# Performance work log

Hardware: AMD Instinct MI355X
Metric: run time of the kernel (lower is better)

## Reference

```python
import jax, jax.numpy as jnp
import numpy as np

N = 100_000   # nodes
E = 1_600_000 # edges
D_IN = 64
HID = 512
OUT = 64
NSEG = HID // OUT  # 8
P = [0, 1, 2]
BN_EPS = 1e-5


def setup_inputs() -> dict:
    key = jax.random.key(0)
    ks = jax.random.split(key, 16)
    feats = jax.random.normal(ks[0], (N, D_IN), dtype=jnp.float32)
    src = jax.random.randint(ks[1], (E,), 0, N, dtype=jnp.int32)
    dst = jax.random.randint(ks[2], (E,), 0, N, dtype=jnp.int32)
    s_in = 1.0 / np.sqrt(D_IN)
    s_fc = 1.0 / np.sqrt(HID * len(P))
    W0 = jax.random.uniform(ks[3], (HID, D_IN), jnp.float32, -s_in, s_in)
    b0 = jnp.zeros((HID,), jnp.float32)
    W1 = jax.random.uniform(ks[4], (HID, D_IN), jnp.float32, -s_in, s_in)
    b1 = jnp.zeros((HID,), jnp.float32)
    W2 = jax.random.uniform(ks[5], (HID, D_IN), jnp.float32, -s_in, s_in)
    b2 = jnp.zeros((HID,), jnp.float32)
    fc_W = jax.random.uniform(ks[6], (HID, HID * len(P)), jnp.float32, -s_fc, s_fc)
    fc_b = jnp.zeros((HID,), jnp.float32)
    gamma = jnp.ones((HID,), jnp.float32)
    beta = jnp.zeros((HID,), jnp.float32)
    q = jax.random.uniform(ks[7], (NSEG,), jnp.float32)
    return dict(feats=feats, src=src, dst=dst, W0=W0, b0=b0, W1=W1, b1=b1,
                W2=W2, b2=b2, fc_W=fc_W, fc_b=fc_b, gamma=gamma, beta=beta, q=q)


def _mixhop_layer(feats, src, dst, Ws, bs, fc_W, fc_b, gamma, beta):
    # degree norm: deg^{-1/2}, clamped at 1
    deg = jax.ops.segment_sum(jnp.ones((E,), feats.dtype), dst, num_segments=N)
    norm = jnp.clip(deg, 1.0, None) ** -0.5  # [N]
    norm = norm[:, None]
    outputs = []
    h = feats
    for j in range(max(P) + 1):
        h = h * norm
        # SpMM: sum over incoming edges (copy_u + sum)
        h = jax.ops.segment_sum(h[src], dst, num_segments=N)
        h = h * norm
        if j in P:
            outputs.append(h @ Ws[j].T + bs[j])  # [N, HID]
    cat = jnp.concatenate(outputs, axis=1)       # [N, 3*HID]
    final = cat @ fc_W.T + fc_b                  # [N, HID]
    # BatchNorm1d (training-mode batch statistics, biased var)
    mu = jnp.mean(final, axis=0)
    var = jnp.mean((final - mu) ** 2, axis=0)
    final = (final - mu) * jax.lax.rsqrt(var + BN_EPS) * gamma + beta
    return final


def reference(feats, src, dst, W0, b0, W1, b1, W2, b2, fc_W, fc_b, gamma, beta, q):
    h = _mixhop_layer(feats, src, dst, [W0, W1, W2], [b0, b1, b2],
                      fc_W, fc_b, gamma, beta)           # [N, HID]
    # segment mixing: sum_k q[k] * h[:, k*OUT:(k+1)*OUT]
    out = jnp.einsum('nko,k->no', h.reshape(N, NSEG, OUT), q)  # [N, OUT]
    return out
```

## Files before the change

kernel.cpp:

```cpp
#include <hip/hip_runtime.h>
#include <hip/hip_bf16.h>
#include <stdint.h>

typedef unsigned short ushort;
typedef unsigned int uint;
typedef unsigned char uchar;

#define N_NODES 100000
#define N_EDGES 1600000
#define KDIM 192
#define HIDDEN 512
#define NCHUNK 782
#define NCH 2
#define NPART 391
#define SDIM (KDIM*KDIM)
#define NPAIR 78
#define PPB   9984
#define NSPLIT 8
#define LDT 194
#define NSLICE 256
#define EPS (N_EDGES/NSLICE)

#define NB 391
#define BCAP 5120

typedef __attribute__((ext_vector_type(8))) short short8;
typedef __attribute__((ext_vector_type(4))) short short4v;
typedef __attribute__((ext_vector_type(4))) uint uint4v;
typedef __attribute__((ext_vector_type(4))) float float4v;
typedef __attribute__((ext_vector_type(2))) float float2v;
typedef __attribute__((ext_vector_type(2))) uint uint2v;

__device__ __forceinline__ float bf2f(ushort u){
    uint x = ((uint)u) << 16;
    return __builtin_bit_cast(float, x);
}
__device__ __forceinline__ float bflo(uint u){
    return __builtin_bit_cast(float, u << 16);
}
__device__ __forceinline__ float bfhi(uint u){
    return __builtin_bit_cast(float, u & 0xffff0000u);
}
__device__ __forceinline__ ushort f2bf(float f){
    uint u = __builtin_bit_cast(uint, f);
    u += 0x7fffu + ((u >> 16) & 1u);
    return (ushort)(u >> 16);
}

__global__ __launch_bounds__(1024) void k_histA(const int* __restrict__ dst,
                                                uint* __restrict__ histA){
    __shared__ uint cnt[NB];
    int slice = blockIdx.x, t = threadIdx.x;
    for (int b = t; b < NB; b += 1024) cnt[b] = 0;
    __syncthreads();
    int e0 = slice * EPS;
    for (int i = t; i < EPS; i += 1024){
        uint d = (uint)dst[e0 + i];
        atomicAdd(&cnt[d >> 8], 1u);
    }
    __syncthreads();
    for (int b = t; b < NB; b += 1024) histA[(size_t)b*NSLICE + slice] = cnt[b];
}

__global__ void k_scanSl(const uint* __restrict__ histA, uint* __restrict__ sbase,
                         uint* __restrict__ btot){
    __shared__ uint sc[NSLICE];
    int b = blockIdx.x, t = threadIdx.x;
    uint v = histA[(size_t)b*NSLICE + t];
    sc[t] = v; __syncthreads();
    for (int off = 1; off < 256; off <<= 1){
        uint u = (t >= off) ? sc[t - off] : 0;
        __syncthreads();
        sc[t] += u;
        __syncthreads();
    }
    sbase[(size_t)b*NSLICE + t] = sc[t] - v;
    if (t == 255) btot[b] = sc[255];
}

__global__ void k_scanBk(const uint* __restrict__ btot, uint* __restrict__ bstart){
    __shared__ uint sc[512];
    int t = threadIdx.x;
    uint v = (t < NB) ? btot[t] : 0;
    sc[t] = v; __syncthreads();
    for (int off = 1; off < 512; off <<= 1){
        uint u = (t >= off) ? sc[t - off] : 0;
        __syncthreads();
        sc[t] += u;
        __syncthreads();
    }
    if (t < NB) bstart[t] = sc[t] - v;
}

__global__ __launch_bounds__(1024) void k_packA(const int* __restrict__ src,
                                                const int* __restrict__ dst,
                                                const uint* __restrict__ sbase,
                                                const uint* __restrict__ bstart,
                                                uint* __restrict__ rec){
    __shared__ uint arr[NB];
    int slice = blockIdx.x, t = threadIdx.x;
    for (int b = t; b < NB; b += 1024)
        arr[b] = bstart[b] + sbase[(size_t)b*NSLICE + slice];
    __syncthreads();
    int e0 = slice * EPS;
    for (int i = t; i < EPS; i += 1024){
        int e = e0 + i;
        uint d = (uint)dst[e];
        uint bk = d >> 8;
        uint slot = atomicAdd(&arr[bk], 1u);
        rec[slot] = (uint)src[e] | ((d & 255u) << 17);
    }
}

__global__ __launch_bounds__(256) void k_passB(const uint* __restrict__ rec,
                                               const uint* __restrict__ bstart,
                                               const uint* __restrict__ btot,
                                               const float* __restrict__ feats,
                                               int* __restrict__ csr,
                                               int* __restrict__ deg,
                                               int* __restrict__ rowptr,
                                               float* __restrict__ nrm,
                                               ushort* __restrict__ Hx){
    __shared__ uint recs[BCAP];
    __shared__ uint cntL[256];
    __shared__ uint ofs[256];
    __shared__ float nrmL[256];
    int b = blockIdx.x, t = threadIdx.x;
    uint base = bstart[b], cnt = btot[b];
    cntL[t] = 0;
    __syncthreads();
    for (uint i = t; i < cnt; i += 256){
        uint rv = rec[base + i];
        if (i < BCAP) recs[i] = rv;
        atomicAdd(&cntL[(rv >> 17) & 255u], 1u);
    }
    __syncthreads();
    uint c = cntL[t];
    ofs[t] = c; __syncthreads();
    for (int off = 1; off < 256; off <<= 1){
        uint u = (t >= off) ? ofs[t - off] : 0;
        __syncthreads();
        ofs[t] += u;
        __syncthreads();
    }
    uint excl = ofs[t] - c;
    int node = b*256 + t;
    float nv = rsqrtf((float)(c > 0 ? c : 1));
    nrmL[t] = nv;
    if (node < N_NODES){
        deg[node] = (int)c;
        rowptr[node] = (int)(base + excl);
        nrm[node] = nv;
    }
    __syncthreads();
    ofs[t] = excl;
    __syncthreads();
    for (uint i = t; i < cnt; i += 256){
        uint rv = (i < BCAP) ? recs[i] : rec[base + i];
        uint n = (rv >> 17) & 255u;
        uint p = atomicAdd(&ofs[n], 1u);
        csr[base + p] = (int)(rv & 0x1FFFFu);
    }
    int nodeBase = b*256;
    for (int g = t; g < 256*16; g += 256){
        int ln = g >> 4;
        int nd = nodeBase + ln;
        if (nd < N_NODES){
            float w = nrmL[ln];
            float4v v = ((const float4v*)feats)[(long)nd*16 + (g & 15)];
            short4v o;
            o[0] = (short)f2bf(v[0]*w); o[1] = (short)f2bf(v[1]*w);
            o[2] = (short)f2bf(v[2]*w); o[3] = (short)f2bf(v[3]*w);
            ((short4v*)Hx)[(long)nd*16 + (g & 15)] = o;
        }
    }
}

template<bool WRITE_HS>
__global__ __launch_bounds__(256, 4) void k_agg(const ushort* __restrict__ inp,
                      ushort* __restrict__ H, int outoff,
                      ushort* __restrict__ Hs,
                      const int* __restrict__ rowptr, const int* __restrict__ deg,
                      const float* __restrict__ nrm, const int* __restrict__ csr){
    int node = (blockIdx.x << 3) + (threadIdx.x >> 5);
    int lane = threadIdx.x & 63;
    if (node >= N_NODES) return;
    int slot = (lane & 31) >> 3;
    int fb   = lane & 7;
    int beg = rowptr[node];
    int d   = deg[node];
    float acc[8] = {};
    if (d > 0 && d <= 32){
        int emax = beg + d - 1;
        int idx[8];
        #pragma unroll
        for (int k = 0; k < 8; ++k){
            int e = beg + slot + k*4;
            idx[k] = csr[e < emax ? e : emax];
        }
        uint4v v[8];
        #pragma unroll
        for (int k = 0; k < 8; ++k)
            v[k] = *(const uint4v*)(inp + (long)idx[k]*64 + fb*8);
        #pragma unroll
        for (int k = 0; k < 8; ++k){
            if (slot + k*4 < d){
                #pragma unroll
                for (int p = 0; p < 4; ++p){
                    acc[2*p]   += bflo(v[k][p]);
                    acc[2*p+1] += bfhi(v[k][p]);
                }
            }
        }
    } else if (d > 32){
        int i = 0;
        for (; i + 8 <= d; i += 8){
            int sA = csr[beg + i + slot];
            int sB = csr[beg + i + 4 + slot];
            uint4v vA = *(const uint4v*)(inp + (long)sA*64 + fb*8);
            uint4v vB = *(const uint4v*)(inp + (long)sB*64 + fb*8);
            #pragma unroll
            for (int p = 0; p < 4; ++p){
                acc[2*p]   += bflo(vA[p]); acc[2*p+1] += bfhi(vA[p]);
                acc[2*p]   += bflo(vB[p]); acc[2*p+1] += bfhi(vB[p]);
            }
        }
        if (i + 4 <= d){
            int sA = csr[beg + i + slot];
            uint4v vA = *(const uint4v*)(inp + (long)sA*64 + fb*8);
            #pragma unroll
            for (int p = 0; p < 4; ++p){
                acc[2*p]   += bflo(vA[p]); acc[2*p+1] += bfhi(vA[p]);
            }
            i += 4;
        }
        if (i + slot < d){
            int s = csr[beg + i + slot];
            uint4v v = *(const uint4v*)(inp + (long)s*64 + fb*8);
            #pragma unroll
            for (int p = 0; p < 4; ++p){
                acc[2*p]   += bflo(v[p]); acc[2*p+1] += bfhi(v[p]);
            }
        }
    }
    #pragma unroll
    for (int k = 0; k < 8; ++k){
        acc[k] += __shfl_xor(acc[k], 8);
        acc[k] += __shfl_xor(acc[k], 16);
    }
    if (slot == 0){
        float wn = nrm[node];
        short8 o;
        #pragma unroll
        for (int k = 0; k < 8; ++k) o[k] = (short)f2bf(wn * acc[k]);
        *(short8*)(H + (long)node*KDIM + outoff + fb*8) = o;
        if (WRITE_HS){
            float w2 = wn * wn;
            short8 o2;
            #pragma unroll
            for (int k = 0; k < 8; ++k) o2[k] = (short)f2bf(w2 * acc[k]);
            *(short8*)(Hs + (long)node*64 + fb*8) = o2;
        }
    }
}

__global__ __launch_bounds__(192) void k_prepM1(const float* __restrict__ W0,
                                                const float* __restrict__ W1,
                                                const float* __restrict__ W2,
                                                const float* __restrict__ fcW,
                                                float* __restrict__ MTp){
    int ks = blockIdx.x;
    int c0 = blockIdx.y * 4;
    int jd = threadIdx.x;
    int j = jd >> 6, d = jd & 63;
    const float* W  = (j == 0) ? W0 : (j == 1) ? W1 : W2;
    const float* wp = W + (ks*64)*64 + d;
    const float* f0 = fcW + (long)(c0+0)*1536 + j*512 + ks*64;
    const float* f1 = fcW + (long)(c0+1)*1536 + j*512 + ks*64;
    const float* f2 = fcW + (long)(c0+2)*1536 + j*512 + ks*64;
    const float* f3 = fcW + (long)(c0+3)*1536 + j*512 + ks*64;
    float a0 = 0.f, a1 = 0.f, a2 = 0.f, a3 = 0.f;
    #pragma unroll 8
    for (int k = 0; k < 64; ++k){
        float w = wp[k*64];
        a0 += w * f0[k]; a1 += w * f1[k]; a2 += w * f2[k]; a3 += w * f3[k];
    }
    long base = (long)ks*(HIDDEN*KDIM) + (long)c0*KDIM + jd;
    MTp[base]         = a0;
    MTp[base + KDIM]  = a1;
    MTp[base + 2*KDIM]= a2;
    MTp[base + 3*KDIM]= a3;
}

__global__ void k_prepM2(const float* __restrict__ MTp, ushort* __restrict__ MT){
    int i = blockIdx.x*256 + threadIdx.x;
    if (i >= HIDDEN*KDIM) return;
    float s = 0.f;
    #pragma unroll
    for (int ks = 0; ks < 8; ++ks) s += MTp[(long)ks*(HIDDEN*KDIM) + i];
    MT[i] = f2bf(s);
}

__global__ __launch_bounds__(256) void k_bias(const float* __restrict__ b0,
                                              const float* __restrict__ b1,
                                              const float* __restrict__ b2,
                                              const float* __restrict__ fcW,
                                              const float* __restrict__ fcb,
                                              float* __restrict__ Bc){
    __shared__ float red[256];
    int c = blockIdx.x, t = threadIdx.x;
    const float* fw = fcW + (long)c*1536;
    float s = b0[t]*fw[t]          + b0[t+256]*fw[t+256]
            + b1[t]*fw[512+t]      + b1[t+256]*fw[512+t+256]
            + b2[t]*fw[1024+t]     + b2[t+256]*fw[1024+t+256];
    red[t] = s; __syncthreads();
    for (int off = 128; off > 0; off >>= 1){
        if (t < off) red[t] += red[t + off];
        __syncthreads();
    }
    if (t == 0) Bc[c] = fcb[c] + red[0];
}

template<int W>
__device__ __forceinline__ void do_pairs(const short8* frag, float4v* acc){
    int p = 0, c = 0;
    #pragma unroll
    for (int i = 0; i < 12; ++i)
        #pragma unroll
        for (int j = i; j < 12; ++j){
            if ((p & 3) == W){
                acc[c] = __builtin_amdgcn_mfma_f32_16x16x32_bf16(frag[i], frag[j], acc[c], 0,0,0);
                ++c;
            }
            ++p;
        }
}
template<int W>
__device__ __forceinline__ void store_pairs(const float4v* acc, uint* Pb, int lane){
    int p = 0, c = 0;
    #pragma unroll
    for (int i = 0; i < 12; ++i)
        #pragma unroll
        for (int j = i; j < 12; ++j){
            if ((p & 3) == W){
                uint2v v;
                v[0] = (uint)f2bf(acc[c][0]) | ((uint)f2bf(acc[c][1]) << 16);
                v[1] = (uint)f2bf(acc[c][2]) | ((uint)f2bf(acc[c][3]) << 16);
                *(uint2v*)(Pb + p*128 + lane*2) = v;
                ++c;
            }
            ++p;
        }
}

__global__ __launch_bounds__(256, 2) void k_hth(const ushort* __restrict__ H,
                                                uint* __restrict__ P,
                                                float* __restrict__ msum){
    __shared__ ushort Ts[128*LDT];
    int t = threadIdx.x;
    int w = t >> 6, lane = t & 63;
    int m16 = lane & 15, quad = lane >> 4;
    float4v acc[20] = {};
    #pragma unroll
    for (int cc = 0; cc < NCH; ++cc){
        int chunk = blockIdx.x * NCH + cc;
        int n0 = chunk * 128;
        #pragma unroll
        for (int it = 0; it < 12; ++it){
            int flat = it*256 + t;
            int row = flat / 24, seg = flat - row*24;
            int gr = n0 + row;
            short8 v = {0,0,0,0,0,0,0,0};
            if (gr < N_NODES) v = *(const short8*)(H + (long)gr*KDIM + seg*8);
            *(short8*)(Ts + row*LDT + seg*8) = v;
        }
        __syncthreads();
        #pragma unroll
        for (int kt = 0; kt < 4; ++kt){
            short8 frag[12];
            #pragma unroll
            for (int b = 0; b < 12; ++b){
                short8 f;
                #pragma unroll
                for (int j = 0; j < 8; ++j)
                    f[j] = (short)Ts[(kt*32 + quad*8 + j)*LDT + b*16 + m16];
                frag[b] = f;
            }
            if      (w == 0) do_pairs<0>(frag, acc);
            else if (w == 1) do_pairs<1>(frag, acc);
            else if (w == 2) do_pairs<2>(frag, acc);
            else             do_pairs<3>(frag, acc);
        }
        if (t < KDIM){
            float s = 0.f;
            #pragma unroll 4
            for (int n = 0; n < 128; ++n) s += bf2f(Ts[n*LDT + t]);
            atomicAdd(&msum[t], s);
        }
        __syncthreads();
    }
    uint* Pb = P + (long)blockIdx.x * PPB;
    if      (w == 0) store_pairs<0>(acc, Pb, lane);
    else if (w == 1) store_pairs<1>(acc, Pb, lane);
    else if (w == 2) store_pairs<2>(acc, Pb, lane);
    else             store_pairs<3>(acc, Pb, lane);
}

__global__ void k_reduce(const uint* __restrict__ P, float* __restrict__ SP){
    int p = blockIdx.x * 256 + threadIdx.x;
    int y = blockIdx.y;
    int b0 = y * 49, b1 = min(b0 + 49, NPART);
    float lo = 0.f, hi = 0.f;
    for (int b = b0; b < b1; ++b){
        uint v = P[(long)b*PPB + p];
        lo += bf2f((ushort)(v & 0xffff));
        hi += bf2f((ushort)(v >> 16));
    }
    float2v o; o[0] = lo; o[1] = hi;
    *(float2v*)(SP + (long)y*(NPAIR*256) + p*2) = o;
}

__global__ void k_finC(const float* __restrict__ SP, const float* __restrict__ msum,
                       float* __restrict__ C){
    int idx = blockIdx.x * 256 + threadIdx.x;
    float s = 0.f;
    #pragma unroll
    for (int y = 0; y < NSPLIT; ++y) s += SP[(long)y*(NPAIR*256) + idx];
    int h = idx & 1, pu = idx >> 1;
    int p = pu >> 7, rem = pu & 127;
    int l = rem >> 1, u = rem & 1;
    int r = u*2 + h;
    int pi = 0, pj = 0, off = 0;
    #pragma unroll
    for (int k = 0; k < 12; ++k){
        int len = 12 - k;
        if (p >= off && p < off + len){ pi = k; pj = k + (p - off); }
        off += len;
    }
    int m = pi*16 + (l >> 4)*4 + r;
    int n = pj*16 + (l & 15);
    const float invN = 1.f / (float)N_NODES;
    float v = s*invN - (msum[m]*invN)*(msum[n]*invN);
    C[m*KDIM + n] = v;
    C[n*KDIM + m] = v;
}

__global__ __launch_bounds__(192) void k_cv1(const float* __restrict__ C,
                                             const ushort* __restrict__ MT,
                                             float* __restrict__ Vp){
    int ks = blockIdx.x;
    int c0 = blockIdx.y * 4;
    int d  = threadIdx.x;
    const ushort* m0 = MT + (long)(c0+0)*KDIM + ks*48;
    const ushort* m1 = MT + (long)(c0+1)*KDIM + ks*48;
    const ushort* m2 = MT + (long)(c0+2)*KDIM + ks*48;
    const ushort* m3 = MT + (long)(c0+3)*KDIM + ks*48;
    const float* cp = C + (long)(ks*48)*KDIM + d;
    float a0 = 0.f, a1 = 0.f, a2 = 0.f, a3 = 0.f;
    #pragma unroll 8
    for (int k = 0; k < 48; ++k){
        float cv = cp[(long)k*KDIM];
        a0 += bf2f(m0[k]) * cv; a1 += bf2f(m1[k]) * cv;
        a2 += bf2f(m2[k]) * cv; a3 += bf2f(m3[k]) * cv;
    }
    long base = (long)ks*(HIDDEN*KDIM) + (long)c0*KDIM + d;
    Vp[base]          = a0;
    Vp[base + KDIM]   = a1;
    Vp[base + 2*KDIM] = a2;
    Vp[base + 3*KDIM] = a3;
}

__global__ __launch_bounds__(192) void k_solveA(const float* __restrict__ Vp,
                                                const ushort* __restrict__ MT,
                                                const float* __restrict__ msum,
                                                const float* __restrict__ Bc,
                                                const float* __restrict__ gamma,
                                                const float* __restrict__ beta,
                                                float* __restrict__ rr,
                                                float* __restrict__ tmpBN){
    __shared__ float redM[192];
    __shared__ float redV[192];
    int c = blockIdx.x, d = threadIdx.x;
    const float invN = 1.f / (float)N_NODES;
    float m = bf2f(MT[(long)c*KDIM + d]);
    long vi = (long)c*KDIM + d;
    float vsum = Vp[vi] + Vp[vi + HIDDEN*KDIM] + Vp[vi + 2*HIDDEN*KDIM]
               + Vp[vi + 3*HIDDEN*KDIM];
    redM[d] = msum[d]*invN * m;
    redV[d] = vsum * m;
    __syncthreads();
    for (int off = 96; off >= 3; off >>= 1){
        if (d < off){ redM[d] += redM[d + off]; redV[d] += redV[d + off]; }
        __syncthreads();
    }
    if (d == 0){
        float mu  = Bc[c] + redM[0] + redM[1] + redM[2];
        float var = redV[0] + redV[1] + redV[2];
        float r = gamma[c] * rsqrtf(var + 1e-5f);
        rr[c] = r;
        tmpBN[c] = r * (Bc[c] - mu) + beta[c];
    }
}

__global__ void k_buildG(const ushort* __restrict__ MT, const float* __restrict__ rr,
                         const float* __restrict__ q, const float* __restrict__ tmpBN,
                         ushort* __restrict__ GT, float* __restrict__ cvec){
    int o = blockIdx.x, d = threadIdx.x;
    float s = 0.f;
    #pragma unroll
    for (int k = 0; k < 8; ++k)
        s += q[k] * rr[k*64 + o] * bf2f(MT[(k*64 + o)*KDIM + d]);
    GT[o*KDIM + d] = f2bf(s);
    if (o == 0 && d < 64){
        float cs = 0.f;
        #pragma unroll
        for (int k = 0; k < 8; ++k) cs += q[k] * tmpBN[k*64 + d];
        cvec[d] = cs;
    }
}

#define LDA 200
__global__ __launch_bounds__(256) void k_outgemm(const ushort* __restrict__ H,
                                                 const ushort* __restrict__ GT,
                                                 const float* __restrict__ cvec,
                                                 float* __restrict__ out){
    __shared__ ushort As[128*LDA];
    __shared__ ushort Gs[64*LDA];
    int t = threadIdx.x;
    int n0 = blockIdx.x * 128;
    int w = t >> 6, lane = t & 63;
    int m16 = lane & 15, quad = lane >> 4;
    int wr = w * 32;
    float4v acc[2][4] = {};
    #pragma unroll
    for (int it = 0; it < 12; ++it){
        int flat = it*256 + t;
        int row = flat / 24, seg = flat - row*24;
        int gr = n0 + row;
        short8 v = {0,0,0,0,0,0,0,0};
        if (gr < N_NODES) v = *(const short8*)(H + (long)gr*KDIM + seg*8);
        *(short8*)(As + row*LDA + seg*8) = v;
    }
    #pragma unroll
    for (int it = 0; it < 6; ++it){
        int flat = it*256 + t;
        int row = flat / 24, seg = flat - row*24;
        short8 v = *(const short8*)(GT + row*KDIM + seg*8);
        *(short8*)(Gs + row*LDA + seg*8) = v;
    }
    __syncthreads();
    #pragma unroll
    for (int kk = 0; kk < 192; kk += 32){
        short8 af[2], bf[4];
        #pragma unroll
        for (int i = 0; i < 2; ++i)
            af[i] = *(const short8*)(As + (wr + i*16 + m16)*LDA + kk + quad*8);
        #pragma unroll
        for (int j = 0; j < 4; ++j)
            bf[j] = *(const short8*)(Gs + (j*16 + m16)*LDA + kk + quad*8);
        #pragma unroll
        for (int i = 0; i < 2; ++i)
            #pragma unroll
            for (int j = 0; j < 4; ++j)
                acc[i][j] = __builtin_amdgcn_mfma_f32_16x16x32_bf16(af[i], bf[j], acc[i][j], 0,0,0);
    }
    #pragma unroll
    for (int i = 0; i < 2; ++i)
        #pragma unroll
        for (int j = 0; j < 4; ++j)
            #pragma unroll
            for (int r = 0; r < 4; ++r){
                int rowg = n0 + wr + i*16 + quad*4 + r;
                int o = j*16 + m16;
                if (rowg < N_NODES) out[(long)rowg*64 + o] = acc[i][j][r] + cvec[o];
            }
}

extern "C" void kernel_launch(void* const* d_in, const int* in_sizes, int n_in,
                              void* d_out, int out_size, void* d_ws, size_t ws_size,
                              hipStream_t stream) {
    const float* feats = (const float*)d_in[0];
    const int*   src   = (const int*)  d_in[1];
    const int*   dst   = (const int*)  d_in[2];
    const float* W0    = (const float*)d_in[3];
    const float* b0    = (const float*)d_in[4];
    const float* W1    = (const float*)d_in[5];
    const float* b1    = (const float*)d_in[6];
    const float* W2    = (const float*)d_in[7];
    const float* b2    = (const float*)d_in[8];
    const float* fcW   = (const float*)d_in[9];
    const float* fcb   = (const float*)d_in[10];
    const float* gamma = (const float*)d_in[11];
    const float* beta  = (const float*)d_in[12];
    const float* q     = (const float*)d_in[13];
    float* out = (float*)d_out;

    char* ws = (char*)d_ws;
    size_t off = 0;
    auto alloc = [&](size_t bytes) -> char* {
        char* p = ws + off;
        off = (off + bytes + 511) & ~(size_t)511;
        return p;
    };
    uint*   histA   = (uint*)  alloc((size_t)NB * NSLICE * 4);
    uint*   sbase   = (uint*)  alloc((size_t)NB * NSLICE * 4);
    uint*   btot    = (uint*)  alloc((size_t)NB * 4);
    uint*   bstart  = (uint*)  alloc((size_t)NB * 4);
    uint*   rec     = (uint*)  alloc((size_t)N_EDGES * 4);
    int*    deg     = (int*)   alloc((size_t)N_NODES * 4);
    int*    rowptr  = (int*)   alloc((size_t)N_NODES * 4);
    float*  nrm     = (float*) alloc((size_t)N_NODES * 4);
    int*    csr     = (int*)   alloc((size_t)N_EDGES * 4);
    ushort* Hx      = (ushort*)alloc((size_t)N_NODES * 64 * 2);
    ushort* HsB     = (ushort*)alloc((size_t)N_NODES * 64 * 2);
    ushort* H       = (ushort*)alloc((size_t)N_NODES * KDIM * 2);
    ushort* MT      = (ushort*)alloc((size_t)HIDDEN * KDIM * 2);
    float*  MTp     = (float*) alloc((size_t)8 * HIDDEN * KDIM * 4);
    float*  Bc      = (float*) alloc((size_t)HIDDEN * 4);
    float*  msum    = (float*) alloc((size_t)KDIM * 4);
    uint*   P       = (uint*)  alloc((size_t)NPART * PPB * 4);
    float*  SP      = (float*) alloc((size_t)NSPLIT * NPAIR * 256 * 4);
    float*  C       = (float*) alloc((size_t)SDIM * 4);
    float*  Vp      = (float*) alloc((size_t)4 * HIDDEN * KDIM * 4);
    float*  rr      = (float*) alloc((size_t)HIDDEN * 4);
    float*  tmpBN   = (float*) alloc((size_t)HIDDEN * 4);
    float*  cvec    = (float*) alloc((size_t)64 * 4);
    ushort* GT      = (ushort*)alloc((size_t)64 * KDIM * 2);
    (void)ws_size; (void)n_in; (void)in_sizes; (void)out_size;

    hipMemsetAsync(msum, 0, (size_t)KDIM * 4, stream);

    k_histA <<<NSLICE, 1024, 0, stream>>>(dst, histA);
    k_scanSl<<<NB, 256, 0, stream>>>(histA, sbase, btot);
    k_scanBk<<<1, 512, 0, stream>>>(btot, bstart);
    k_packA <<<NSLICE, 1024, 0, stream>>>(src, dst, sbase, bstart, rec);
    k_passB <<<NB, 256, 0, stream>>>(rec, bstart, btot, feats, csr, deg, rowptr, nrm, Hx);

    int aggGrid = (N_NODES + 7) / 8;
    k_agg<true> <<<aggGrid, 256, 0, stream>>>(Hx,  H, 0,   HsB, rowptr, deg, nrm, csr);
    k_agg<true> <<<aggGrid, 256, 0, stream>>>(HsB, H, 64,  Hx,  rowptr, deg, nrm, csr);
    k_agg<false><<<aggGrid, 256, 0, stream>>>(Hx,  H, 128, HsB, rowptr, deg, nrm, csr);

    dim3 pmGrid(8, HIDDEN/4);
    k_prepM1<<<pmGrid, 192, 0, stream>>>(W0, W1, W2, fcW, MTp);
    k_prepM2<<<(HIDDEN*KDIM + 255)/256, 256, 0, stream>>>(MTp, MT);
    k_bias <<<HIDDEN, 256, 0, stream>>>(b0, b1, b2, fcW, fcb, Bc);

    k_hth   <<<NPART, 256, 0, stream>>>(H, P, msum);
    dim3 rGrid(PPB/256, NSPLIT);
    k_reduce<<<rGrid, 256, 0, stream>>>(P, SP);
    k_finC  <<<NPAIR, 256, 0, stream>>>(SP, msum, C);
    dim3 cvGrid(4, HIDDEN/4);
    k_cv1   <<<cvGrid, 192, 0, stream>>>(C, MT, Vp);
    k_solveA<<<HIDDEN, 192, 0, stream>>>(Vp, MT, msum, Bc, gamma, beta, rr, tmpBN);
    k_buildG<<<64, KDIM, 0, stream>>>(MT, rr, q, tmpBN, GT, cvec);

    k_outgemm<<<NCHUNK, 256, 0, stream>>>(H, GT, cvec, out);
}
```

Baseline: 350.0 us.

## Slice gather features into four 16-column planes for cache-local SpMM aggregation

Stores the bf16 node features as four separate 16-column slices, each a contiguous [N,16] plane, and launches the aggregation kernel over four times as many blocks. Each block handles one slice. One node is now served by 16 edge slots times 2 feature lanes instead of 4 slots times 8 lanes. Each gather plane is about 3.2 MB, so it can stay resident in cache while its slice is processed, and each node issues more independent edge loads at once. The cost is that csr and rowptr are re-read four times, there are more shuffle reductions, and each gathered row is only 32 bytes.

Result: slower. 485.2 us (+38.6%).

```diff
diff --git a/kernel.cpp b/kernel.cpp
--- a/kernel.cpp
+++ b/kernel.cpp
@@ -167,11 +167,13 @@
         int nd = nodeBase + ln;
         if (nd < N_NODES){
             float w = nrmL[ln];
-            float4v v = ((const float4v*)feats)[(long)nd*16 + (g & 15)];
+            int q = g & 15;
+            float4v v = ((const float4v*)feats)[(long)nd*16 + q];
             short4v o;
             o[0] = (short)f2bf(v[0]*w); o[1] = (short)f2bf(v[1]*w);
             o[2] = (short)f2bf(v[2]*w); o[3] = (short)f2bf(v[3]*w);
-            ((short4v*)Hx)[(long)nd*16 + (g & 15)] = o;
+            int sl = q >> 2;
+            ((short4v*)Hx)[(long)sl*(N_NODES*4) + (long)nd*4 + (q & 3)] = o;
         }
     }
 }
@@ -182,84 +184,68 @@
                       ushort* __restrict__ Hs,
                       const int* __restrict__ rowptr, const int* __restrict__ deg,
                       const float* __restrict__ nrm, const int* __restrict__ csr){
-    int node = (blockIdx.x << 3) + (threadIdx.x >> 5);
-    int lane = threadIdx.x & 63;
-    if (node >= N_NODES) return;
-    int slot = (lane & 31) >> 3;
-    int fb   = lane & 7;
+    int s    = blockIdx.x & 3;
+    int node = (blockIdx.x >> 2)*8 + (threadIdx.x >> 5);
+    int l    = threadIdx.x & 31;
+    int flane = l & 1;
+    int slot  = l >> 1;
     int beg = rowptr[node];
     int d   = deg[node];
+    const ushort* T = inp + (long)s*(N_NODES*16);
     float acc[8] = {};
-    if (d > 0 && d <= 32){
+    if (d > 0){
         int emax = beg + d - 1;
-        int idx[8];
-        #pragma unroll
-        for (int k = 0; k < 8; ++k){
-            int e = beg + slot + k*4;
-            idx[k] = csr[e < emax ? e : emax];
-        }
-        uint4v v[8];
-        #pragma unroll
-        for (int k = 0; k < 8; ++k)
-            v[k] = *(const uint4v*)(inp + (long)idx[k]*64 + fb*8);
-        #pragma unroll
-        for (int k = 0; k < 8; ++k){
-            if (slot + k*4 < d){
+        int e0 = beg + slot;
+        int id0 = csr[e0 < emax ? e0 : emax];
+        uint4v v0 = *(const uint4v*)(T + (long)id0*16 + flane*8);
+        uint4v v1 = {};
+        if (d > 16){
+            int e1 = beg + 16 + slot;
+            int id1 = csr[e1 < emax ? e1 : emax];
+            v1 = *(const uint4v*)(T + (long)id1*16 + flane*8);
+        }
+        if (slot < d){
+            #pragma unroll
+            for (int p = 0; p < 4; ++p){
+                acc[2*p]   += bflo(v0[p]); acc[2*p+1] += bfhi(v0[p]);
+            }
+        }
+        if (16 + slot < d){
+            #pragma unroll
+            for (int p = 0; p < 4; ++p){
+                acc[2*p]   += bflo(v1[p]); acc[2*p+1] += bfhi(v1[p]);
+            }
+        }
+        for (int i = 32; i < d; i += 16){
+            if (i + slot < d){
+                int idt = csr[beg + i + slot];
+                uint4v vt = *(const uint4v*)(T + (long)idt*16 + flane*8);
                 #pragma unroll
                 for (int p = 0; p < 4; ++p){
-                    acc[2*p]   += bflo(v[k][p]);
-                    acc[2*p+1] += bfhi(v[k][p]);
+                    acc[2*p]   += bflo(vt[p]); acc[2*p+1] += bfhi(vt[p]);
                 }
             }
         }
-    } else if (d > 32){
-        int i = 0;
-        for (; i + 8 <= d; i += 8){
-            int sA = csr[beg + i + slot];
-            int sB = csr[beg + i + 4 + slot];
-            uint4v vA = *(const uint4v*)(inp + (long)sA*64 + fb*8);
-            uint4v vB = *(const uint4v*)(inp + (long)sB*64 + fb*8);
-            #pragma unroll
-            for (int p = 0; p < 4; ++p){
-                acc[2*p]   += bflo(vA[p]); acc[2*p+1] += bfhi(vA[p]);
-                acc[2*p]   += bflo(vB[p]); acc[2*p+1] += bfhi(vB[p]);
-            }
-        }
-        if (i + 4 <= d){
-            int sA = csr[beg + i + slot];
-            uint4v vA = *(const uint4v*)(inp + (long)sA*64 + fb*8);
-            #pragma unroll
-            for (int p = 0; p < 4; ++p){
-                acc[2*p]   += bflo(vA[p]); acc[2*p+1] += bfhi(vA[p]);
-            }
-            i += 4;
-        }
-        if (i + slot < d){
-            int s = csr[beg + i + slot];
-            uint4v v = *(const uint4v*)(inp + (long)s*64 + fb*8);
-            #pragma unroll
-            for (int p = 0; p < 4; ++p){
-                acc[2*p]   += bflo(v[p]); acc[2*p+1] += bfhi(v[p]);
-            }
-        }
     }
     #pragma unroll
     for (int k = 0; k < 8; ++k){
+        acc[k] += __shfl_xor(acc[k], 2);
+        acc[k] += __shfl_xor(acc[k], 4);
         acc[k] += __shfl_xor(acc[k], 8);
         acc[k] += __shfl_xor(acc[k], 16);
     }
-    if (slot == 0){
+    if (l < 2){
         float wn = nrm[node];
         short8 o;
         #pragma unroll
         for (int k = 0; k < 8; ++k) o[k] = (short)f2bf(wn * acc[k]);
-        *(short8*)(H + (long)node*KDIM + outoff + fb*8) = o;
+        *(short8*)(H + (long)node*KDIM + outoff + s*16 + flane*8) = o;
         if (WRITE_HS){
             float w2 = wn * wn;
             short8 o2;
             #pragma unroll
             for (int k = 0; k < 8; ++k) o2[k] = (short)f2bf(w2 * acc[k]);
-            *(short8*)(Hs + (long)node*64 + fb*8) = o2;
+            *(short8*)(Hs + (long)s*(N_NODES*16) + (long)node*16 + flane*8) = o2;
         }
     }
 }
@@ -636,7 +622,7 @@
     k_packA <<<NSLICE, 1024, 0, stream>>>(src, dst, sbase, bstart, rec);
     k_passB <<<NB, 256, 0, stream>>>(rec, bstart, btot, feats, csr, deg, rowptr, nrm, Hx);
 
-    int aggGrid = (N_NODES + 7) / 8;
+    int aggGrid = (N_NODES / 8) * 4;
     k_agg<true> <<<aggGrid, 256, 0, stream>>>(Hx,  H, 0,   HsB, rowptr, deg, nrm, csr);
     k_agg<true> <<<aggGrid, 256, 0, stream>>>(HsB, H, 64,  Hx,  rowptr, deg, nrm, csr);
     k_agg<false><<<aggGrid, 256, 0, stream>>>(Hx,  H, 128, HsB, rowptr, deg, nrm, csr);
```
